# Kernel optimization log

Measured on AMD Instinct MI355X. Metric: run time of the kernel, lower is better.

## Reference

```python
import jax, jax.numpy as jnp
import numpy as np

B, V, J, NB, NPCA = 16384, 778, 16, 10, 6
PARENTS = np.array([-1, 0, 1, 2, 0, 4, 5, 0, 7, 8, 0, 10, 11, 0, 13, 14])


def setup_inputs() -> dict:
    key = jax.random.key(0)
    ks = jax.random.split(key, 12)
    return {
        "betas": jax.random.normal(ks[0], (B, NB)) * 0.5,
        "global_orient": jax.random.normal(ks[1], (B, 3)) * 0.3,
        "hand_pose": jax.random.normal(ks[2], (B, NPCA)) * 0.5,
        "transl": jax.random.normal(ks[3], (B, 3)) * 0.1,
        "hand_components": jax.random.normal(ks[4], (NPCA, 45)) * 0.3,
        "pose_mean": jax.random.normal(ks[5], (48,)) * 0.05,
        "v_template": jax.random.normal(ks[6], (V, 3)) * 0.05,
        "shapedirs": jax.random.normal(ks[7], (V, 3, NB)) * 0.01,
        "posedirs": jax.random.normal(ks[8], (135, V * 3)) * 0.01,
        "J_regressor": jax.nn.softmax(jax.random.normal(ks[9], (J, V)), axis=-1),
        "lbs_weights": jax.nn.softmax(jax.random.normal(ks[10], (V, J)) * 4.0, axis=-1),
        "parents": jnp.asarray(PARENTS, dtype=jnp.int32),
    }


def _rodrigues(rot_vecs):
    # rot_vecs: [B, J, 3] axis-angle -> [B, J, 3, 3] rotation matrices
    angle = jnp.linalg.norm(rot_vecs + 1e-8, axis=-1, keepdims=True)  # [B,J,1]
    axis = rot_vecs / angle
    rx, ry, rz = axis[..., 0], axis[..., 1], axis[..., 2]
    z = jnp.zeros_like(rx)
    K = jnp.stack([z, -rz, ry, rz, z, -rx, -ry, rx, z], axis=-1).reshape(rx.shape + (3, 3))
    sin = jnp.sin(angle)[..., None]
    cos = jnp.cos(angle)[..., None]
    I3 = jnp.eye(3, dtype=rot_vecs.dtype)
    return I3 + sin * K + (1.0 - cos) * jnp.matmul(K, K)


def reference(betas, global_orient, hand_pose, transl, hand_components, pose_mean,
              v_template, shapedirs, posedirs, J_regressor, lbs_weights, parents):
    dtype = betas.dtype
    # PCA -> full axis-angle pose, add pose mean
    full_pose = jnp.concatenate([global_orient, hand_pose @ hand_components], axis=1) + pose_mean  # [B,48]

    v_shaped = v_template + jnp.einsum('bl,vkl->bvk', betas, shapedirs)      # [B,V,3]
    joints = jnp.einsum('jv,bvk->bjk', J_regressor, v_shaped)                # [B,J,3]

    # pose blendshapes
    rot_mats = _rodrigues(full_pose.reshape(-1, J, 3))                        # [B,J,3,3]
    I3 = jnp.eye(3, dtype=dtype)
    pose_feature = (rot_mats[:, 1:] - I3).reshape(-1, (J - 1) * 9)            # [B,135]
    v_posed = v_shaped + (pose_feature @ posedirs).reshape(-1, V, 3)          # [B,V,3]

    # kinematic chain (parents are static model constants)
    par = np.asarray(parents)
    rel_joints = jnp.concatenate([joints[:, :1], joints[:, 1:] - joints[:, par[1:]]], axis=1)
    top = jnp.concatenate([rot_mats, rel_joints[..., None]], axis=-1)         # [B,J,3,4]
    bottom = jnp.broadcast_to(jnp.array([0., 0., 0., 1.], dtype=dtype), top.shape[:2] + (1, 4))
    transforms_mat = jnp.concatenate([top, bottom], axis=2)                   # [B,J,4,4]

    chain = [transforms_mat[:, 0]]
    for i in range(1, J):
        chain.append(chain[par[i]] @ transforms_mat[:, i])
    transforms = jnp.stack(chain, axis=1)                                     # [B,J,4,4]
    posed_joints = transforms[..., :3, 3]                                     # [B,J,3]

    # remove rest-pose joint locations -> relative transforms A
    joints_hom = jnp.concatenate([joints, jnp.zeros_like(joints[..., :1])], axis=-1)  # [B,J,4]
    init_bone = jnp.einsum('bjmn,bjn->bjm', transforms, joints_hom)           # [B,J,4]
    rel_transforms = transforms - jnp.pad(init_bone[..., None], ((0, 0), (0, 0), (0, 0), (3, 0)))

    # linear blend skinning
    T = jnp.einsum('vj,bjmn->bvmn', lbs_weights, rel_transforms)              # [B,V,4,4]
    v_hom = jnp.concatenate([v_posed, jnp.ones_like(v_posed[..., :1])], axis=-1)
    vertices = jnp.einsum('bvmn,bvn->bvm', T, v_hom)[..., :3]                 # [B,V,3]

    vertices = vertices + transl[:, None]
    posed_joints = posed_joints + transl[:, None]
    return vertices, posed_joints
```

## Files before the change

kernel.cpp:

```cpp
#include <hip/hip_runtime.h>
#include <hip/hip_bf16.h>


typedef __hip_bfloat16 bf16;
typedef unsigned short u16;
typedef unsigned int u32;
typedef __attribute__((ext_vector_type(8))) short short8;
typedef __attribute__((ext_vector_type(4))) float f32x4;

#define BATCH 16384
#define NVERT 778
#define NJOINT 16
#define NSHAPE 10
#define NPCA 6
#define NPF 135
#define PD_COLS (NVERT * 3)
#define VERT_ELEMS ((size_t)BATCH * NVERT * 3)
#define BB 32
#define NBLK (BATCH / BB)
#define NSUPER 49
#define NCTILE 147
#define NCHUNK 34
#define PDT_CHUNKS 36
#define PDT_ELEMS (PDT_CHUNKS * PD_COLS * 4)
#define MT_ELEMS (NCTILE * 5 * 64 * 8)
#define PDT_BYTE_OFF 4096
#define TRELP 196

__device__ __forceinline__ float b2f(bf16 x) { return __bfloat162float(x); }
__device__ __forceinline__ bf16  f2b(float x) { return __float2bfloat16(x); }

__device__ __forceinline__ int parent_of(int j) {
    return (j == 0) ? -1 : (((j - 1) % 3 == 0) ? 0 : j - 1);
}

template <typename T> __device__ __forceinline__ float ldv(const void* p, size_t i);
template <> __device__ __forceinline__ float ldv<float>(const void* p, size_t i) {
    return ((const float*)p)[i];
}
template <> __device__ __forceinline__ float ldv<bf16>(const void* p, size_t i) {
    return b2f(((const bf16*)p)[i]);
}

template <typename T> __device__ __forceinline__ void stv(void* p, size_t i, float v);
template <> __device__ __forceinline__ void stv<float>(void* p, size_t i, float v) {
    ((float*)p)[i] = v;
}
template <> __device__ __forceinline__ void stv<bf16>(void* p, size_t i, float v) {
    ((bf16*)p)[i] = f2b(v);
}

__device__ __forceinline__ u16 bf_bits(float x) {
    union { bf16 h; u16 u; } cvt;
    cvt.h = f2b(x);
    return cvt.u;
}
__device__ __forceinline__ float bflo(u32 u) {
    union { u32 i; float f; } t; t.i = u << 16; return t.f;
}
__device__ __forceinline__ float bfhi(u32 u) {
    union { u32 i; float f; } t; t.i = u & 0xffff0000u; return t.f;
}

__global__ void detect_dtype(const u16* __restrict__ betas_u, int* __restrict__ flag) {
    __shared__ int s_cnt[256];
    int tid = threadIdx.x;
    int cnt = 0;
    for (int i = tid; i < BATCH * NSHAPE; i += 256) {
        int e = (betas_u[i] >> 7) & 0xFF;
        cnt += (e >= 134) ? 1 : 0;
    }
    s_cnt[tid] = cnt;
    __syncthreads();
    for (int s = 128; s > 0; s >>= 1) {
        if (tid < s) s_cnt[tid] += s_cnt[tid + s];
        __syncthreads();
    }
    if (tid == 0) *flag = (s_cnt[0] > 1000) ? 1 : 0;
}

template <typename T>
__device__ void precompute_body(const void* Jreg, const void* v_template,
                                const void* shapedirs, float* jt, float* jsd) {
    int idx = blockIdx.x * blockDim.x + threadIdx.x;
    if (idx >= 48 + 480) return;
    if (idx < 48) {
        int j = idx / 3, k = idx % 3;
        float acc = 0.f;
        for (int v = 0; v < NVERT; ++v)
            acc += ldv<T>(Jreg, j * NVERT + v) * ldv<T>(v_template, v * 3 + k);
        jt[idx] = acc;
    } else {
        int o = idx - 48;
        int jk = o / NSHAPE, l = o % NSHAPE;
        int j = jk / 3, k = jk % 3;
        float acc = 0.f;
        for (int v = 0; v < NVERT; ++v)
            acc += ldv<T>(Jreg, j * NVERT + v) * ldv<T>(shapedirs, (v * 3 + k) * NSHAPE + l);
        jsd[o] = acc;
    }
}

__global__ void precompute_kernel(const void* Jreg, const void* v_template,
                                  const void* shapedirs, const int* __restrict__ flag,
                                  float* jt, float* jsd) {
    if (*flag) precompute_body<float>(Jreg, v_template, shapedirs, jt, jsd);
    else       precompute_body<bf16 >(Jreg, v_template, shapedirs, jt, jsd);
}

__device__ void transpose_f32(const float* pd, float* pdT) {
    int idx = blockIdx.x * blockDim.x + threadIdx.x;
    if (idx >= PDT_ELEMS) return;
    int j = idx & 3;
    int rc = idx >> 2;
    int r = rc % PD_COLS;
    int c = rc / PD_COLS;
    int p = c * 4 + j;
    pdT[idx] = (p < NPF) ? pd[(size_t)p * PD_COLS + r] : 0.f;
}

__device__ void transpose_mfma(const u16* pdu, const u16* sdu, const u16* vtu,
                               u16* out) {
    int idx = blockIdx.x * blockDim.x + threadIdx.x;
    if (idx >= MT_ELEMS) return;
    int i  = idx & 7;
    int l  = (idx >> 3) & 63;
    int u  = idx >> 9;
    int ks = u % 5, t = u / 5;
    int k   = ks * 32 + ((l >> 4) << 3) + i;
    int col = t * 16 + (l & 15);
    u16 bits = 0;
    if (col < PD_COLS) {
        if (k < NPF)                     bits = pdu[(size_t)k * PD_COLS + col];
        else if (k < NPF + NSHAPE)       bits = sdu[(size_t)col * NSHAPE + (k - NPF)];
        else if (k == NPF + NSHAPE)      bits = vtu[col];
    }
    out[idx] = bits;
}

__global__ void transpose_kernel(const void* pd, const void* sd, const void* vt,
                                 const int* __restrict__ flag, void* pdT) {
    if (*flag) transpose_f32((const float*)pd, (float*)pdT);
    else       transpose_mfma((const u16*)pd, (const u16*)sd, (const u16*)vt,
                              (u16*)pdT);
}

struct __align__(16) SmemB {
    union {
        float pff[16][144];
        u16   pfA[32][168];
    } pf;
    float trel[BB * TRELP];
    union {
        float joints[BB][NJOINT][3];
        float ldsC[4][16][52];
        float ob[4][4][192];
    } c;
    float beta[BB][NSHAPE];
    float transl[BB][3];
    float hp[BB][NPCA];
};

template <typename T>
__device__ void stage1(const void* betas, const void* orient,
                       const void* hand_pose, const void* transl,
                       const void* hc, const void* pose_mean,
                       const float* __restrict__ jt, const float* __restrict__ jsd,
                       int b0s, int ro, void* out_base, SmemB& s) {
    const int tid = threadIdx.x;

    if (tid < 160) {
        int q = tid / NSHAPE, l = tid % NSHAPE;
        s.beta[ro + q][l] = ldv<T>(betas, (size_t)(b0s + q) * NSHAPE + l);
    } else if (tid < 208) {
        int o = tid - 160;
        int q = o / 3, k = o % 3;
        s.transl[ro + q][k] = ldv<T>(transl, (size_t)(b0s + q) * 3 + k);
    } else {
        int o = tid - 208;
        #pragma unroll
        for (int rep = 0; rep < 2; ++rep) {
            int oo = o + rep * 48;
            int q = oo / NPCA, c = oo % NPCA;
            s.hp[ro + q][c] = ldv<T>(hand_pose, (size_t)(b0s + q) * NPCA + c);
        }
    }
    __syncthreads();

    const int bb = tid >> 4;
    const int j  = tid & 15;
    const int rb = ro + bb;
    float R[9];
    float jx[3];
    {
        float p0, p1, p2;
        if (j == 0) {
            const int b = b0s + bb;
            p0 = ldv<T>(orient, (size_t)b * 3 + 0) + ldv<T>(pose_mean, 0);
            p1 = ldv<T>(orient, (size_t)b * 3 + 1) + ldv<T>(pose_mean, 1);
            p2 = ldv<T>(orient, (size_t)b * 3 + 2) + ldv<T>(pose_mean, 2);
        } else {
            int base = 3 * (j - 1);
            p0 = ldv<T>(pose_mean, 3 * j + 0);
            p1 = ldv<T>(pose_mean, 3 * j + 1);
            p2 = ldv<T>(pose_mean, 3 * j + 2);
            #pragma unroll
            for (int c = 0; c < NPCA; ++c) {
                float hpv = s.hp[rb][c];
                p0 += hpv * ldv<T>(hc, c * 45 + base + 0);
                p1 += hpv * ldv<T>(hc, c * 45 + base + 1);
                p2 += hpv * ldv<T>(hc, c * 45 + base + 2);
            }
        }

        float r0 = p0 + 1e-8f, r1 = p1 + 1e-8f, r2 = p2 + 1e-8f;
        float angle = sqrtf(r0 * r0 + r1 * r1 + r2 * r2);
        float inv = 1.f / angle;
        float ax = p0 * inv, ay = p1 * inv, az = p2 * inv;
        float sn = sinf(angle);
        float cc1 = 1.f - cosf(angle);
        R[0] = 1.f + cc1 * (-az * az - ay * ay);
        R[1] = -sn * az + cc1 * ax * ay;
        R[2] =  sn * ay + cc1 * ax * az;
        R[3] =  sn * az + cc1 * ax * ay;
        R[4] = 1.f + cc1 * (-az * az - ax * ax);
        R[5] = -sn * ax + cc1 * ay * az;
        R[6] = -sn * ay + cc1 * ax * az;
        R[7] =  sn * ax + cc1 * ay * az;
        R[8] = 1.f + cc1 * (-ax * ax - ay * ay);

        #pragma unroll
        for (int k = 0; k < 3; ++k) {
            float acc = jt[j * 3 + k];
            #pragma unroll
            for (int l = 0; l < NSHAPE; ++l)
                acc += jsd[(j * 3 + k) * NSHAPE + l] * s.beta[rb][l];
            jx[k] = acc;
            s.c.joints[rb][j][k] = acc;
        }
    }
    __syncthreads();

    {
        int par = parent_of(j);
        float* tm = &s.trel[(size_t)rb * TRELP + j * 12];
        #pragma unroll
        for (int m = 0; m < 3; ++m) {
            float t = jx[m] - (j > 0 ? s.c.joints[rb][par][m] : 0.f);
            tm[m * 4 + 0] = R[m * 3 + 0];
            tm[m * 4 + 1] = R[m * 3 + 1];
            tm[m * 4 + 2] = R[m * 3 + 2];
            tm[m * 4 + 3] = t;
        }
    }
    __syncthreads();

    float G[12];
    {
        int stack[3];
        int depth = 0;
        int i = j;
        while (i != 0 && depth < 3) { stack[depth++] = i; i = parent_of(i); }
        const float* base = &s.trel[(size_t)rb * TRELP];
        #pragma unroll
        for (int t = 0; t < 12; ++t) G[t] = base[t];
        for (int d = depth - 1; d >= 0; --d) {
            const float* Tc = base + stack[d] * 12;
            float Gn[12];
            #pragma unroll
            for (int m = 0; m < 3; ++m) {
                #pragma unroll
                for (int n = 0; n < 4; ++n) {
                    float acc = G[m * 4 + 0] * Tc[0 * 4 + n] +
                                G[m * 4 + 1] * Tc[1 * 4 + n] +
                                G[m * 4 + 2] * Tc[2 * 4 + n];
                    if (n == 3) acc += G[m * 4 + 3];
                    Gn[m * 4 + n] = acc;
                }
            }
            #pragma unroll
            for (int t = 0; t < 12; ++t) G[t] = Gn[t];
        }
    }
    __syncthreads();

    {
        size_t jo = VERT_ELEMS + ((size_t)(b0s + bb) * NJOINT + j) * 3;
        stv<T>(out_base, jo + 0, G[0 * 4 + 3] + s.transl[rb][0]);
        stv<T>(out_base, jo + 1, G[1 * 4 + 3] + s.transl[rb][1]);
        stv<T>(out_base, jo + 2, G[2 * 4 + 3] + s.transl[rb][2]);

        float* rl = &s.trel[(size_t)rb * TRELP + j * 12];
        #pragma unroll
        for (int m = 0; m < 3; ++m) {
            float rbv = G[m * 4 + 3] -
                        (G[m * 4 + 0] * jx[0] + G[m * 4 + 1] * jx[1] + G[m * 4 + 2] * jx[2]);
            rl[m * 4 + 0] = G[m * 4 + 0];
            rl[m * 4 + 1] = G[m * 4 + 1];
            rl[m * 4 + 2] = G[m * 4 + 2];
            rl[m * 4 + 3] = rbv;
        }

        if constexpr (sizeof(T) == 2) {
            u16* pa = &s.pf.pfA[rb][0];
            if (j > 0) {
                u16* po = pa + (j - 1) * 9;
                po[0] = bf_bits(R[0] - 1.f); po[1] = bf_bits(R[1]);       po[2] = bf_bits(R[2]);
                po[3] = bf_bits(R[3]);       po[4] = bf_bits(R[4] - 1.f); po[5] = bf_bits(R[5]);
                po[6] = bf_bits(R[6]);       po[7] = bf_bits(R[7]);       po[8] = bf_bits(R[8] - 1.f);
            } else {
                #pragma unroll
                for (int l2 = 0; l2 < NSHAPE; ++l2)
                    pa[NPF + l2] = bf_bits(s.beta[rb][l2]);
                pa[NPF + NSHAPE] = 0x3F80;
                #pragma unroll
                for (int z = NPF + NSHAPE + 1; z < 168; ++z) pa[z] = 0;
            }
        } else {
            float* pa = s.pf.pff[bb];
            if (j > 0) {
                float* po = pa + (j - 1) * 9;
                po[0] = R[0] - 1.f; po[1] = R[1];       po[2] = R[2];
                po[3] = R[3];       po[4] = R[4] - 1.f; po[5] = R[5];
                po[6] = R[6];       po[7] = R[7];       po[8] = R[8] - 1.f;
            } else {
                #pragma unroll
                for (int z = NPF; z < 144; ++z) pa[z] = 0.f;
            }
        }
    }
    __syncthreads();
}

__device__ __forceinline__ void lbs_epi(const void* lbsw, int b0, int h, int sp,
                                        void* out_base, SmemB& s,
                                        float (*ldsC)[52], int l) {
    const int lb = l & 15, vg = l >> 4;
    asm volatile("s_waitcnt lgkmcnt(0)" ::: "memory");
    __builtin_amdgcn_sched_barrier(0);

    float a4[4][3];
    #pragma unroll
    for (int vv = 0; vv < 4; ++vv)
        #pragma unroll
        for (int cc = 0; cc < 3; ++cc)
            a4[vv][cc] = ldsC[lb][(vg * 4 + vv) * 3 + cc];

    uint4 wr[4][2];
    #pragma unroll
    for (int vv = 0; vv < 4; ++vv) {
        int v = sp * 16 + vg * 4 + vv;
        if (v > NVERT - 1) v = NVERT - 1;
        const uint4* wp = (const uint4*)((const u16*)lbsw + (size_t)v * NJOINT);
        wr[vv][0] = wp[0];
        wr[vv][1] = wp[1];
    }

    const float* relb = &s.trel[(size_t)(h * 16 + lb) * TRELP];
    float Tm[4][12];
    #pragma unroll
    for (int vv = 0; vv < 4; ++vv)
        #pragma unroll
        for (int q = 0; q < 12; ++q) Tm[vv][q] = 0.f;

    #pragma unroll
    for (int jj = 0; jj < NJOINT; ++jj) {
        const float4 r0 = *(const float4*)(relb + jj * 12 + 0);
        const float4 r1 = *(const float4*)(relb + jj * 12 + 4);
        const float4 r2 = *(const float4*)(relb + jj * 12 + 8);
        #pragma unroll
        for (int vv = 0; vv < 4; ++vv) {
            const uint4 wu = wr[vv][(jj >> 3) & 1];
            const int wc = (jj >> 1) & 3;
            const u32 ww = (wc == 0) ? wu.x : (wc == 1) ? wu.y : (wc == 2) ? wu.z : wu.w;
            const float wj = (jj & 1) ? bfhi(ww) : bflo(ww);
            Tm[vv][0] += wj * r0.x; Tm[vv][1]  += wj * r0.y; Tm[vv][2]  += wj * r0.z; Tm[vv][3]  += wj * r0.w;
            Tm[vv][4] += wj * r1.x; Tm[vv][5]  += wj * r1.y; Tm[vv][6]  += wj * r1.z; Tm[vv][7]  += wj * r1.w;
            Tm[vv][8] += wj * r2.x; Tm[vv][9]  += wj * r2.y; Tm[vv][10] += wj * r2.z; Tm[vv][11] += wj * r2.w;
        }
    }

    const float t0 = s.transl[h * 16 + lb][0];
    const float t1 = s.transl[h * 16 + lb][1];
    const float t2 = s.transl[h * 16 + lb][2];
    float o[4][3];
    #pragma unroll
    for (int vv = 0; vv < 4; ++vv) {
        o[vv][0] = Tm[vv][0] * a4[vv][0] + Tm[vv][1] * a4[vv][1] + Tm[vv][2]  * a4[vv][2] + Tm[vv][3]  + t0;
        o[vv][1] = Tm[vv][4] * a4[vv][0] + Tm[vv][5] * a4[vv][1] + Tm[vv][6]  * a4[vv][2] + Tm[vv][7]  + t1;
        o[vv][2] = Tm[vv][8] * a4[vv][0] + Tm[vv][9] * a4[vv][1] + Tm[vv][10] * a4[vv][2] + Tm[vv][11] + t2;
    }

    u32* row = (u32*)&ldsC[lb][0];
    row[vg * 6 + 0] = (u32)bf_bits(o[0][0]) | ((u32)bf_bits(o[0][1]) << 16);
    row[vg * 6 + 1] = (u32)bf_bits(o[0][2]) | ((u32)bf_bits(o[1][0]) << 16);
    row[vg * 6 + 2] = (u32)bf_bits(o[1][1]) | ((u32)bf_bits(o[1][2]) << 16);
    row[vg * 6 + 3] = (u32)bf_bits(o[2][0]) | ((u32)bf_bits(o[2][1]) << 16);
    row[vg * 6 + 4] = (u32)bf_bits(o[2][2]) | ((u32)bf_bits(o[3][0]) << 16);
    row[vg * 6 + 5] = (u32)bf_bits(o[3][1]) | ((u32)bf_bits(o[3][2]) << 16);

    asm volatile("s_waitcnt lgkmcnt(0)" ::: "memory");
    __builtin_amdgcn_sched_barrier(0);

    const int maxw = (sp == NSUPER - 1) ? 15 : 24;
    #pragma unroll
    for (int it = 0; it < 6; ++it) {
        const int i = it * 64 + l;
        const int bb2 = i / 24, c2 = i - bb2 * 24;
        if (c2 < maxw) {
            const u32 val = ((const u32*)&ldsC[bb2][0])[c2];
            *(u32*)((char*)out_base + (size_t)(b0 + h * 16 + bb2) * (NVERT * 3 * 2)
                    + (size_t)sp * 96 + (size_t)c2 * 4) = val;
        }
    }
}

__device__ void mfma_stage2(const u16* __restrict__ pdTm, const void* lbsw,
                            int b0, void* out_base, SmemB& s) {
    const int tid = threadIdx.x;
    const int wv = tid >> 6, l = tid & 63;
    const int lb = l & 15, lq = l >> 4;
    float (*ldsC)[52] = s.c.ldsC[wv];

    for (int sp = wv; sp < NSUPER; sp += 4) {
        short8 afr0[5], afr1[5];
        #pragma unroll
        for (int ks = 0; ks < 5; ++ks) {
            afr0[ks] = *(const short8*)&s.pf.pfA[lb][ks * 32 + lq * 8];
            afr1[ks] = *(const short8*)&s.pf.pfA[16 + lb][ks * 32 + lq * 8];
        }
        f32x4 acc1[3];
        #pragma unroll
        for (int tt = 0; tt < 3; ++tt) {
            const int t = sp * 3 + tt;
            f32x4 a0 = {0.f, 0.f, 0.f, 0.f};
            f32x4 a1 = {0.f, 0.f, 0.f, 0.f};
            #pragma unroll
            for (int ks = 0; ks < 5; ++ks) {
                const short8 bfr = *(const short8*)(pdTm + (((size_t)t * 5 + ks) * 64 + l) * 8);
                a0 = __builtin_amdgcn_mfma_f32_16x16x32_bf16(afr0[ks], bfr, a0, 0, 0, 0);
                a1 = __builtin_amdgcn_mfma_f32_16x16x32_bf16(afr1[ks], bfr, a1, 0, 0, 0);
            }
            #pragma unroll
            for (int r = 0; r < 4; ++r) ldsC[lq * 4 + r][tt * 16 + lb] = a0[r];
            acc1[tt] = a1;
        }
        lbs_epi(lbsw, b0, 0, sp, out_base, s, ldsC, l);
        #pragma unroll
        for (int tt = 0; tt < 3; ++tt)
            #pragma unroll
            for (int r = 0; r < 4; ++r) ldsC[lq * 4 + r][tt * 16 + lb] = acc1[tt][r];
        lbs_epi(lbsw, b0, 1, sp, out_base, s, ldsC, l);
    }
}

template <typename T, bool TRP>
__device__ void vector_stage2(const void* v_template, const void* shapedirs,
                              const void* posedirs, const void* lbsw,
                              const void* __restrict__ pdTv,
                              int b0s, void* out_base, SmemB& s) {
    const int tid = threadIdx.x;
    const int wv = tid >> 6;
    const int ln = tid & 63;

    for (int iter = 0; iter < 4; ++iter) {
        const int vbase = iter * 256 + wv * 64;
        if (vbase >= NVERT) break;
        const int nv = (NVERT - vbase < 64) ? (NVERT - vbase) : 64;
        const int v  = vbase + ln;
        const int vc = (v < NVERT) ? v : (NVERT - 1);
        const int v3 = vc * 3;

        float a[16][3];
        {
            const float q0 = ldv<T>(v_template, v3 + 0);
            const float q1 = ldv<T>(v_template, v3 + 1);
            const float q2 = ldv<T>(v_template, v3 + 2);
            #pragma unroll
            for (int q = 0; q < 16; ++q) { a[q][0] = q0; a[q][1] = q1; a[q][2] = q2; }
        }

        #pragma unroll
        for (int l = 0; l < NSHAPE; ++l) {
            const float sd0 = ldv<T>(shapedirs, (size_t)vc * 30 + 0 * NSHAPE + l);
            const float sd1 = ldv<T>(shapedirs, (size_t)vc * 30 + 1 * NSHAPE + l);
            const float sd2 = ldv<T>(shapedirs, (size_t)vc * 30 + 2 * NSHAPE + l);
            #pragma unroll
            for (int q = 0; q < 16; ++q) {
                const float be = s.beta[q][l];
                a[q][0] += be * sd0;
                a[q][1] += be * sd1;
                a[q][2] += be * sd2;
            }
        }

        auto fma_chunk = [&](float4 px, float4 py, float4 pz, int c) {
            #pragma unroll
            for (int q = 0; q < 16; ++q) {
                const float4 f = *(const float4*)&s.pf.pff[q][c * 4];
                a[q][0] += f.x * px.x + f.y * px.y + f.z * px.z + f.w * px.w;
                a[q][1] += f.x * py.x + f.y * py.y + f.z * py.z + f.w * py.w;
                a[q][2] += f.x * pz.x + f.y * pz.y + f.z * pz.z + f.w * pz.w;
            }
        };

        if constexpr (TRP && sizeof(T) == 4) {
            const float4* __restrict__ pdT4 = (const float4*)pdTv;
            float4 ax = pdT4[(size_t)0 * PD_COLS + v3 + 0];
            float4 ay = pdT4[(size_t)0 * PD_COLS + v3 + 1];
            float4 az = pdT4[(size_t)0 * PD_COLS + v3 + 2];
            float4 bx = pdT4[(size_t)1 * PD_COLS + v3 + 0];
            float4 by = pdT4[(size_t)1 * PD_COLS + v3 + 1];
            float4 bz = pdT4[(size_t)1 * PD_COLS + v3 + 2];
            #pragma unroll 1
            for (int c = 0; c < NCHUNK; c += 2) {
                const size_t n2 = (size_t)(c + 2) * PD_COLS + v3;
                const size_t n3 = (size_t)(c + 3) * PD_COLS + v3;
                float4 cx = pdT4[n2 + 0], cy = pdT4[n2 + 1], cz = pdT4[n2 + 2];
                float4 dx = pdT4[n3 + 0], dy = pdT4[n3 + 1], dz = pdT4[n3 + 2];
                fma_chunk(ax, ay, az, c);
                fma_chunk(bx, by, bz, c + 1);
                ax = cx; ay = cy; az = cz;
                bx = dx; by = dy; bz = dz;
            }
        } else {
            #pragma unroll 1
            for (int c = 0; c < NCHUNK; ++c) {
                const int p = c * 4;
                float pdx[4], pdy[4], pdz[4];
                #pragma unroll
                for (int qq = 0; qq < 3; ++qq) {
                    pdx[qq] = ldv<T>(posedirs, (size_t)(p + qq) * PD_COLS + v3 + 0);
                    pdy[qq] = ldv<T>(posedirs, (size_t)(p + qq) * PD_COLS + v3 + 1);
                    pdz[qq] = ldv<T>(posedirs, (size_t)(p + qq) * PD_COLS + v3 + 2);
                }
                if (p + 3 < NPF) {
                    pdx[3] = ldv<T>(posedirs, (size_t)(p + 3) * PD_COLS + v3 + 0);
                    pdy[3] = ldv<T>(posedirs, (size_t)(p + 3) * PD_COLS + v3 + 1);
                    pdz[3] = ldv<T>(posedirs, (size_t)(p + 3) * PD_COLS + v3 + 2);
                } else {
                    pdx[3] = 0.f; pdy[3] = 0.f; pdz[3] = 0.f;
                }
                fma_chunk(make_float4(pdx[0], pdx[1], pdx[2], pdx[3]),
                          make_float4(pdy[0], pdy[1], pdy[2], pdy[3]),
                          make_float4(pdz[0], pdz[1], pdz[2], pdz[3]), c);
            }
        }

        float w[NJOINT];
        if constexpr (sizeof(T) == 4) {
            const float4* wl = (const float4*)((const float*)lbsw + (size_t)vc * NJOINT);
            #pragma unroll
            for (int g = 0; g < 4; ++g) {
                const float4 t = wl[g];
                w[g * 4 + 0] = t.x; w[g * 4 + 1] = t.y;
                w[g * 4 + 2] = t.z; w[g * 4 + 3] = t.w;
            }
        } else {
            const uint4* wl = (const uint4*)((const u16*)lbsw + (size_t)vc * NJOINT);
            const uint4 w0 = wl[0], w1 = wl[1];
            w[0]  = bflo(w0.x); w[1]  = bfhi(w0.x);
            w[2]  = bflo(w0.y); w[3]  = bfhi(w0.y);
            w[4]  = bflo(w0.z); w[5]  = bfhi(w0.z);
            w[6]  = bflo(w0.w); w[7]  = bfhi(w0.w);
            w[8]  = bflo(w1.x); w[9]  = bfhi(w1.x);
            w[10] = bflo(w1.y); w[11] = bfhi(w1.y);
            w[12] = bflo(w1.z); w[13] = bfhi(w1.z);
            w[14] = bflo(w1.w); w[15] = bfhi(w1.w);
        }

        const int n32 = (nv * 3 * (int)sizeof(T)) >> 2;
        #pragma unroll 1
        for (int g = 0; g < 4; ++g) {
            #pragma unroll
            for (int qq = 0; qq < 4; ++qq) {
                const int q = g * 4 + qq;
                float Tm[12];
                #pragma unroll
                for (int t = 0; t < 12; ++t) Tm[t] = 0.f;
                #pragma unroll
                for (int jj = 0; jj < NJOINT; ++jj) {
                    const float* rl = &s.trel[(size_t)q * TRELP + jj * 12];
                    const float4 r0 = *(const float4*)(rl + 0);
                    const float4 r1 = *(const float4*)(rl + 4);
                    const float4 r2 = *(const float4*)(rl + 8);
                    const float wj = w[jj];
                    Tm[0] += wj * r0.x; Tm[1]  += wj * r0.y; Tm[2]  += wj * r0.z; Tm[3]  += wj * r0.w;
                    Tm[4] += wj * r1.x; Tm[5]  += wj * r1.y; Tm[6]  += wj * r1.z; Tm[7]  += wj * r1.w;
                    Tm[8] += wj * r2.x; Tm[9]  += wj * r2.y; Tm[10] += wj * r2.z; Tm[11] += wj * r2.w;
                }
                const float o0 = Tm[0] * a[q][0] + Tm[1] * a[q][1] + Tm[2]  * a[q][2] + Tm[3]  + s.transl[q][0];
                const float o1 = Tm[4] * a[q][0] + Tm[5] * a[q][1] + Tm[6]  * a[q][2] + Tm[7]  + s.transl[q][1];
                const float o2 = Tm[8] * a[q][0] + Tm[9] * a[q][1] + Tm[10] * a[q][2] + Tm[11] + s.transl[q][2];
                if constexpr (sizeof(T) == 4) {
                    float* ob = &s.c.ob[wv][qq][0];
                    ob[ln * 3 + 0] = o0;
                    ob[ln * 3 + 1] = o1;
                    ob[ln * 3 + 2] = o2;
                } else {
                    u16* ob = (u16*)&s.c.ob[wv][qq][0];
                    ob[ln * 3 + 0] = bf_bits(o0);
                    ob[ln * 3 + 1] = bf_bits(o1);
                    ob[ln * 3 + 2] = bf_bits(o2);
                }
            }
            #pragma unroll
            for (int qq = 0; qq < 4; ++qq) {
                const int q = g * 4 + qq;
                const u32* src = (const u32*)&s.c.ob[wv][qq][0];
                u32* dst = (u32*)((char*)out_base +
                                  ((size_t)(b0s + q) * NVERT + vbase) * 3 * sizeof(T));
                #pragma unroll
                for (int k = 0; k < 3; ++k) {
                    const int idx = k * 64 + ln;
                    if (idx < n32) dst[idx] = src[idx];
                }
            }
        }
    }
}

template <bool TRP>
__global__ __launch_bounds__(256, 3) void mano_fused(
    const void* betas, const void* orient, const void* hand_pose,
    const void* transl, const void* hc, const void* pose_mean,
    const void* v_template, const void* shapedirs, const void* posedirs,
    const void* lbsw, const int* __restrict__ flag,
    const float* __restrict__ jt, const float* __restrict__ jsd,
    const void* __restrict__ pdT,
    void* out_base) {
    __shared__ SmemB s;
    const int b0 = blockIdx.x * BB;

    if (*flag) {
        #pragma unroll 1
        for (int rep = 0; rep < 2; ++rep) {
            stage1<float>(betas, orient, hand_pose, transl, hc, pose_mean,
                          jt, jsd, b0 + rep * 16, 0, out_base, s);
            vector_stage2<float, TRP>(v_template, shapedirs, posedirs, lbsw,
                                      pdT, b0 + rep * 16, out_base, s);
            __syncthreads();
        }
    } else {
        if constexpr (TRP) {
            stage1<bf16>(betas, orient, hand_pose, transl, hc, pose_mean,
                         jt, jsd, b0, 0, out_base, s);
            stage1<bf16>(betas, orient, hand_pose, transl, hc, pose_mean,
                         jt, jsd, b0 + 16, 16, out_base, s);
            mfma_stage2((const u16*)pdT, lbsw, b0, out_base, s);
        } else {
            #pragma unroll 1
            for (int rep = 0; rep < 2; ++rep) {
                stage1<bf16>(betas, orient, hand_pose, transl, hc, pose_mean,
                             jt, jsd, b0 + rep * 16, 0, out_base, s);
                vector_stage2<bf16, false>(v_template, shapedirs, posedirs, lbsw,
                                           pdT, b0 + rep * 16, out_base, s);
                __syncthreads();
            }
        }
    }
}

extern "C" void kernel_launch(void* const* d_in, const int* in_sizes, int n_in,
                              void* d_out, int out_size, void* d_ws, size_t ws_size,
                              hipStream_t stream) {
    const void* betas      = d_in[0];
    const void* orient     = d_in[1];
    const void* hand_pose  = d_in[2];
    const void* transl     = d_in[3];
    const void* hc         = d_in[4];
    const void* pose_mean  = d_in[5];
    const void* v_template = d_in[6];
    const void* shapedirs  = d_in[7];
    const void* posedirs   = d_in[8];
    const void* Jreg       = d_in[9];
    const void* lbsw       = d_in[10];

    int*   flag = (int*)d_ws;
    float* jt   = (float*)d_ws + 16;
    float* jsd  = (float*)d_ws + 64;
    void*  pdT  = (void*)((char*)d_ws + PDT_BYTE_OFF);

    const bool trp = ws_size >= (size_t)PDT_BYTE_OFF + (size_t)PDT_ELEMS * 4;

    hipLaunchKernelGGL(detect_dtype, dim3(1), dim3(256), 0, stream,
                       (const u16*)betas, flag);
    hipLaunchKernelGGL(precompute_kernel, dim3(3), dim3(192), 0, stream,
                       Jreg, v_template, shapedirs, flag, jt, jsd);
    if (trp) {
        hipLaunchKernelGGL(transpose_kernel, dim3((MT_ELEMS + 255) / 256), dim3(256),
                           0, stream, posedirs, shapedirs, v_template, flag, pdT);
        hipLaunchKernelGGL(mano_fused<true>, dim3(NBLK), dim3(256), 0, stream,
                           betas, orient, hand_pose, transl, hc, pose_mean,
                           v_template, shapedirs, posedirs, lbsw, flag, jt, jsd,
                           pdT, d_out);
    } else {
        hipLaunchKernelGGL(mano_fused<false>, dim3(NBLK), dim3(256), 0, stream,
                           betas, orient, hand_pose, transl, hc, pose_mean,
                           v_template, shapedirs, posedirs, lbsw, flag, jt, jsd,
                           pdT, d_out);
    }
    (void)in_sizes; (void)n_in; (void)out_size; (void)ws_size;
}
```

Measured before the change: 995.7 us.

## Pair super-tiles in MFMA stage to write 192-byte contiguous output rows

The MFMA stage now handles two adjacent 16-vertex super-tiles per loop iteration. Their packed bf16 results stay in registers and are staged together through LDS, so each batch row gets a 192-byte contiguous store instead of two 96-byte ones. This is meant to make global writes more coalesced and cut the number of LDS round-trips and waits. Holding extra result registers raises register pressure, so launch bounds drop from 3 to 2 blocks per SM, which lowers occupancy and gives each wave fewer pairs to balance.

New measurement: 987.5 us. No clear change (-0.8%).

```diff
diff --git a/kernel.cpp b/kernel.cpp
--- a/kernel.cpp
+++ b/kernel.cpp
@@ -19,6 +19,7 @@
 #define BB 32
 #define NBLK (BATCH / BB)
 #define NSUPER 49
+#define NPAIR 25
 #define NCTILE 147
 #define NCHUNK 34
 #define PDT_CHUNKS 36
@@ -332,9 +333,9 @@
     __syncthreads();
 }
 
-__device__ __forceinline__ void lbs_epi(const void* lbsw, int b0, int h, int sp,
-                                        void* out_base, SmemB& s,
-                                        float (*ldsC)[52], int l) {
+__device__ __forceinline__ void lbs_calc(const void* lbsw, int h, int sp,
+                                         SmemB& s, float (*ldsC)[52], int l,
+                                         u32 out6[6]) {
     const int lb = l & 15, vg = l >> 4;
     asm volatile("s_waitcnt lgkmcnt(0)" ::: "memory");
     __builtin_amdgcn_sched_barrier(0);
@@ -391,28 +392,42 @@
         o[vv][2] = Tm[vv][8] * a4[vv][0] + Tm[vv][9] * a4[vv][1] + Tm[vv][10] * a4[vv][2] + Tm[vv][11] + t2;
     }
 
-    u32* row = (u32*)&ldsC[lb][0];
-    row[vg * 6 + 0] = (u32)bf_bits(o[0][0]) | ((u32)bf_bits(o[0][1]) << 16);
-    row[vg * 6 + 1] = (u32)bf_bits(o[0][2]) | ((u32)bf_bits(o[1][0]) << 16);
-    row[vg * 6 + 2] = (u32)bf_bits(o[1][1]) | ((u32)bf_bits(o[1][2]) << 16);
-    row[vg * 6 + 3] = (u32)bf_bits(o[2][0]) | ((u32)bf_bits(o[2][1]) << 16);
-    row[vg * 6 + 4] = (u32)bf_bits(o[2][2]) | ((u32)bf_bits(o[3][0]) << 16);
-    row[vg * 6 + 5] = (u32)bf_bits(o[3][1]) | ((u32)bf_bits(o[3][2]) << 16);
-
-    asm volatile("s_waitcnt lgkmcnt(0)" ::: "memory");
-    __builtin_amdgcn_sched_barrier(0);
-
-    const int maxw = (sp == NSUPER - 1) ? 15 : 24;
+    out6[0] = (u32)bf_bits(o[0][0]) | ((u32)bf_bits(o[0][1]) << 16);
+    out6[1] = (u32)bf_bits(o[0][2]) | ((u32)bf_bits(o[1][0]) << 16);
+    out6[2] = (u32)bf_bits(o[1][1]) | ((u32)bf_bits(o[1][2]) << 16);
+    out6[3] = (u32)bf_bits(o[2][0]) | ((u32)bf_bits(o[2][1]) << 16);
+    out6[4] = (u32)bf_bits(o[2][2]) | ((u32)bf_bits(o[3][0]) << 16);
+    out6[5] = (u32)bf_bits(o[3][1]) | ((u32)bf_bits(o[3][2]) << 16);
+}
+
+__device__ __forceinline__ void super_tile(const u16* __restrict__ pdTm,
+                                           const void* lbsw, int sp,
+                                           const short8* afr0, const short8* afr1,
+                                           SmemB& s, float (*ldsC)[52],
+                                           int l, int lq, int lb,
+                                           u32 rh0[6], u32 rh1[6]) {
+    f32x4 acc1[3];
     #pragma unroll
-    for (int it = 0; it < 6; ++it) {
-        const int i = it * 64 + l;
-        const int bb2 = i / 24, c2 = i - bb2 * 24;
-        if (c2 < maxw) {
-            const u32 val = ((const u32*)&ldsC[bb2][0])[c2];
-            *(u32*)((char*)out_base + (size_t)(b0 + h * 16 + bb2) * (NVERT * 3 * 2)
-                    + (size_t)sp * 96 + (size_t)c2 * 4) = val;
-        }
-    }
+    for (int tt = 0; tt < 3; ++tt) {
+        const int t = sp * 3 + tt;
+        f32x4 a0 = {0.f, 0.f, 0.f, 0.f};
+        f32x4 a1 = {0.f, 0.f, 0.f, 0.f};
+        #pragma unroll
+        for (int ks = 0; ks < 5; ++ks) {
+            const short8 bfr = *(const short8*)(pdTm + (((size_t)t * 5 + ks) * 64 + l) * 8);
+            a0 = __builtin_amdgcn_mfma_f32_16x16x32_bf16(afr0[ks], bfr, a0, 0, 0, 0);
+            a1 = __builtin_amdgcn_mfma_f32_16x16x32_bf16(afr1[ks], bfr, a1, 0, 0, 0);
+        }
+        #pragma unroll
+        for (int r = 0; r < 4; ++r) ldsC[lq * 4 + r][tt * 16 + lb] = a0[r];
+        acc1[tt] = a1;
+    }
+    lbs_calc(lbsw, 0, sp, s, ldsC, l, rh0);
+    #pragma unroll
+    for (int tt = 0; tt < 3; ++tt)
+        #pragma unroll
+        for (int r = 0; r < 4; ++r) ldsC[lq * 4 + r][tt * 16 + lb] = acc1[tt][r];
+    lbs_calc(lbsw, 1, sp, s, ldsC, l, rh1);
 }
 
 __device__ void mfma_stage2(const u16* __restrict__ pdTm, const void* lbsw,
@@ -420,37 +435,51 @@
     const int tid = threadIdx.x;
     const int wv = tid >> 6, l = tid & 63;
     const int lb = l & 15, lq = l >> 4;
+    const int vg = l >> 4;
     float (*ldsC)[52] = s.c.ldsC[wv];
 
-    for (int sp = wv; sp < NSUPER; sp += 4) {
+    for (int p = wv; p < NPAIR; p += 4) {
         short8 afr0[5], afr1[5];
         #pragma unroll
         for (int ks = 0; ks < 5; ++ks) {
             afr0[ks] = *(const short8*)&s.pf.pfA[lb][ks * 32 + lq * 8];
             afr1[ks] = *(const short8*)&s.pf.pfA[16 + lb][ks * 32 + lq * 8];
         }
-        f32x4 acc1[3];
-        #pragma unroll
-        for (int tt = 0; tt < 3; ++tt) {
-            const int t = sp * 3 + tt;
-            f32x4 a0 = {0.f, 0.f, 0.f, 0.f};
-            f32x4 a1 = {0.f, 0.f, 0.f, 0.f};
-            #pragma unroll
-            for (int ks = 0; ks < 5; ++ks) {
-                const short8 bfr = *(const short8*)(pdTm + (((size_t)t * 5 + ks) * 64 + l) * 8);
-                a0 = __builtin_amdgcn_mfma_f32_16x16x32_bf16(afr0[ks], bfr, a0, 0, 0, 0);
-                a1 = __builtin_amdgcn_mfma_f32_16x16x32_bf16(afr1[ks], bfr, a1, 0, 0, 0);
-            }
-            #pragma unroll
-            for (int r = 0; r < 4; ++r) ldsC[lq * 4 + r][tt * 16 + lb] = a0[r];
-            acc1[tt] = a1;
-        }
-        lbs_epi(lbsw, b0, 0, sp, out_base, s, ldsC, l);
-        #pragma unroll
-        for (int tt = 0; tt < 3; ++tt)
-            #pragma unroll
-            for (int r = 0; r < 4; ++r) ldsC[lq * 4 + r][tt * 16 + lb] = acc1[tt][r];
-        lbs_epi(lbsw, b0, 1, sp, out_base, s, ldsC, l);
+
+        u32 r00[6], r01[6], r10[6], r11[6];
+        #pragma unroll
+        for (int k = 0; k < 6; ++k) { r10[k] = 0u; r11[k] = 0u; }
+
+        super_tile(pdTm, lbsw, 2 * p, afr0, afr1, s, ldsC, l, lq, lb, r00, r01);
+        if (p < NPAIR - 1)
+            super_tile(pdTm, lbsw, 2 * p + 1, afr0, afr1, s, ldsC, l, lq, lb, r10, r11);
+
+        const int nw = (p == NPAIR - 1) ? 15 : 48;
+        #pragma unroll
+        for (int h = 0; h < 2; ++h) {
+            const u32* rA = (h == 0) ? r00 : r01;
+            const u32* rB = (h == 0) ? r10 : r11;
+            asm volatile("s_waitcnt lgkmcnt(0)" ::: "memory");
+            __builtin_amdgcn_sched_barrier(0);
+            u32* row = (u32*)&ldsC[lb][0];
+            #pragma unroll
+            for (int k = 0; k < 6; ++k) {
+                row[vg * 6 + k]      = rA[k];
+                row[24 + vg * 6 + k] = rB[k];
+            }
+            asm volatile("s_waitcnt lgkmcnt(0)" ::: "memory");
+            __builtin_amdgcn_sched_barrier(0);
+            #pragma unroll
+            for (int it = 0; it < 12; ++it) {
+                const int i = it * 64 + l;
+                const int bb2 = i / 48, c2 = i - bb2 * 48;
+                if (c2 < nw) {
+                    const u32 val = ((const u32*)&ldsC[bb2][0])[c2];
+                    *(u32*)((char*)out_base + (size_t)(b0 + h * 16 + bb2) * (NVERT * 3 * 2)
+                            + (size_t)p * 192 + (size_t)c2 * 4) = val;
+                }
+            }
+        }
     }
 }
 
@@ -621,7 +650,7 @@
 }
 
 template <bool TRP>
-__global__ __launch_bounds__(256, 3) void mano_fused(
+__global__ __launch_bounds__(256, 2) void mano_fused(
     const void* betas, const void* orient, const void* hand_pose,
     const void* transl, const void* hc, const void* pose_mean,
     const void* v_template, const void* shapedirs, const void* posedirs,
```
